# Performance work log

Hardware: AMD Instinct MI355X
Metric: run time of the kernel (lower is better)

Reference implementation:

```python
import jax, jax.numpy as jnp
import numpy as np

T, B, D, H, N, A = 128, 32, 512, 512, 64, 32  # time, batch, feat, hidden(=entry), mem_cap, anchors
TAU = 1.0

def setup_inputs() -> dict:
    key = jax.random.key(0)
    ks = jax.random.split(key, 12)
    s = 0.08  # init_scale
    u = lambda k, sh: jax.random.uniform(k, sh, jnp.float32, -s, s)
    return {
        "x": jax.random.normal(ks[0], (T, B, D), jnp.float32),
        "length": jax.random.randint(ks[1], (B,), 0, T).astype(jnp.int32),
        "u_noise": jax.random.uniform(ks[2], (T, B, N), jnp.float32),
        "W_ih": u(ks[3], (D, 3 * H)),
        "W_hh": u(ks[4], (H, 3 * H)),
        "bias": jnp.zeros((6 * H,), jnp.float32),
        "W_im": u(ks[5], (D, H)),
        "W_hm": u(ks[6], (H, H)),
        "W_um": u(ks[7], (N, H)),
        "fc1_w": u(ks[8], (H, N)),
        "fc1_b": jnp.zeros((N,), jnp.float32),
        "fc2_w": u(ks[9], (2 * H, H)),
        "fc2_b": jnp.zeros((H,), jnp.float32),
        "fc_w": u(ks[10], (H, A)),
        "fc_b": jnp.zeros((A,), jnp.float32),
    }


def reference(x, length, u_noise, W_ih, W_hh, bias, W_im, W_hm, W_um,
              fc1_w, fc1_b, fc2_w, fc2_b, fc_w, fc_b):
    bias_ih, bias_hh = bias[: 3 * H], bias[3 * H :]

    def step(carry, inp):
        h, mem, usage, last_read = carry  # h:[B,H] mem:[B,N,H] usage,last_read:[B,N]
        x_t, u_t, t = inp
        # --- write h_0 into memory (sequential fill, then overwrite last read slot)
        fill = jnp.broadcast_to(jax.nn.one_hot(t, N, dtype=h.dtype), (B, N))
        w = jnp.where(t < N, fill, last_read)
        mem = mem * (1.0 - w[:, :, None]) + w[:, :, None] * h[:, None, :]
        # --- addressing (inputs detached in original)
        last_use = jax.lax.stop_gradient(jax.nn.sigmoid(usage))
        xd = jax.lax.stop_gradient(x_t)
        hd = jax.lax.stop_gradient(h)
        read_head = jnp.tanh(xd @ W_im + hd @ W_hm + last_use @ W_um) @ fc1_w + fc1_b
        # --- gumbel softmax (hard, straight-through); noise as in original formula
        g = -jnp.log(1e-20 - jnp.log(1e-20 + u_t))
        y = jax.nn.softmax((read_head + g) * TAU, axis=1)
        hard = jax.nn.one_hot(jnp.argmax(y, axis=1), N, dtype=y.dtype)
        y_st = jax.lax.stop_gradient(hard - y) + y
        entry = jnp.einsum('bn,bnh->bh', y_st, mem)  # hard gather w/ ST grad
        # usage: add_(-1) then add_(-usage*read_index) => (usage-1)*(1-read_index)
        usage = jax.lax.stop_gradient((usage - 1.0) * (1.0 - hard))
        # --- GRU-like update with h_new from read entry
        h_new = jnp.concatenate([entry, h], axis=1) @ fc2_w + fc2_b
        wi = x_t @ W_ih + bias_ih
        wh = h_new @ W_hh + bias_hh
        ri, zi, ni = jnp.split(wi, 3, axis=1)
        rh, zh, nh = jnp.split(wh, 3, axis=1)
        r = jax.nn.sigmoid(ri + rh)
        z = jax.nn.sigmoid(zi + zh)
        n = jnp.tanh(ni + r * nh)
        h1 = (1.0 - z) * n + z * h_new
        mask = (t < length).astype(h1.dtype)[:, None]
        h1 = h1 * mask + h * (1.0 - mask)
        return (h1, mem, usage, hard), h1

    carry0 = (
        jnp.zeros((B, H), x.dtype),
        jnp.zeros((B, N, H), x.dtype),
        jnp.full((B, N), -99999.0, x.dtype),
        jnp.zeros((B, N), x.dtype),
    )
    ts = jnp.arange(T)
    _, hs = jax.lax.scan(step, carry0, (x, u_noise, ts))  # hs: [T,B,H]
    return hs @ fc_w + fc_b  # [T,B,A]
```

## Files before the change

### kernel.cpp

```cpp
#include <hip/hip_runtime.h>
#include <hip/hip_bf16.h>
#include <math.h>

#define NTHR  512
#define NBLK  256
#define HTXS  18432

#define OFF_HTX  8192
#define OFF_OC   (OFF_HTX + 129*HTXS)
#define OFF_HNEW (OFF_OC + 32*4608)
#define OFF_WHH  (OFF_HNEW + 32*64*512)
#define OFF_C0   (OFF_WHH + 32*64*1536)
#define OFF_WCAT (OFF_C0 + 1536)
#define OFF_WB16 (OFF_WCAT + 576*4608)
#define OFF_P1   (OFF_WB16 + 512*1536)
#define OFF_P2   (OFF_P1 + 4096*1536)

__device__ __forceinline__ float cohLoad(const float* p) {
  return __hip_atomic_load(p, __ATOMIC_RELAXED, __HIP_MEMORY_SCOPE_AGENT);
}
__device__ __forceinline__ void cohStore(float* p, float v) {
  __hip_atomic_store(p, v, __ATOMIC_RELAXED, __HIP_MEMORY_SCOPE_AGENT);
}
__device__ __forceinline__ int cohLoadI(const int* p) {
  return __hip_atomic_load(p, __ATOMIC_RELAXED, __HIP_MEMORY_SCOPE_AGENT);
}
__device__ __forceinline__ void cohStoreI(int* p, int v) {
  __hip_atomic_store(p, v, __ATOMIC_RELAXED, __HIP_MEMORY_SCOPE_AGENT);
}
__device__ __forceinline__ float bf2f(unsigned short u) {
  return __uint_as_float(((unsigned int)u) << 16);
}

__global__ __launch_bounds__(256) void gemm_f32(
    const float* __restrict__ A, const float* __restrict__ B,
    const float* __restrict__ bias, float* __restrict__ C,
    int M, int N, int K, int lda, int ldb, int ldc)
{
  __shared__ float As[16][132];
  __shared__ float Bs[16][64];
  const int bm = blockIdx.x * 128, bn = blockIdx.y * 64;
  const int tid = threadIdx.x;
  const int tx = tid & 15, ty = tid >> 4;
  float acc[8][4];
  #pragma unroll
  for (int i = 0; i < 8; ++i)
    #pragma unroll
    for (int j = 0; j < 4; ++j) acc[i][j] = 0.f;

  for (int kt = 0; kt < K; kt += 16) {
    #pragma unroll
    for (int i = 0; i < 2; ++i) {
      int li = tid + i*256;
      int r = li >> 2, q = li & 3;
      float4 a4 = *(const float4*)(A + (size_t)(bm + r)*lda + kt + q*4);
      As[q*4+0][r] = a4.x; As[q*4+1][r] = a4.y;
      As[q*4+2][r] = a4.z; As[q*4+3][r] = a4.w;
    }
    {
      int k = tid >> 4, nq = tid & 15;
      *(float4*)(&Bs[k][nq*4]) = *(const float4*)(B + (size_t)(kt + k)*ldb + bn + nq*4);
    }
    __syncthreads();
    #pragma unroll
    for (int kk = 0; kk < 16; ++kk) {
      float av[8], bv[4];
      *(float4*)(av)   = *(const float4*)(&As[kk][ty*8]);
      *(float4*)(av+4) = *(const float4*)(&As[kk][ty*8+4]);
      *(float4*)(bv)   = *(const float4*)(&Bs[kk][tx*4]);
      #pragma unroll
      for (int i = 0; i < 8; ++i)
        #pragma unroll
        for (int j = 0; j < 4; ++j) acc[i][j] += av[i]*bv[j];
    }
    __syncthreads();
  }
  #pragma unroll
  for (int i = 0; i < 8; ++i) {
    int m = bm + ty*8 + i;
    #pragma unroll
    for (int j = 0; j < 4; ++j) {
      int n = bn + tx*4 + j;
      float v = acc[i][j];
      if (bias) v += bias[n];
      C[(size_t)m*ldc + n] = v;
    }
  }
}

__global__ __launch_bounds__(512) void setup_kernel(
    const float* __restrict__ W_hm, const float* __restrict__ fc2_w,
    const float* __restrict__ W_um, const float* __restrict__ W_hh,
    const float* __restrict__ bias, const float* __restrict__ fc2_b,
    float* __restrict__ Wcat, float* __restrict__ c0)
{
  const int idx = blockIdx.x * 512 + threadIdx.x;
  if (idx < 512*1536) {
    int k = idx / 1536, c = idx % 1536;
    float v;
    if (c < 512)       v = W_hm[k*512 + c];
    else if (c < 1024) v = fc2_w[k*512 + (c-512)];
    else               v = fc2_w[(size_t)(512+k)*512 + (c-1024)];
    Wcat[(size_t)k*4608 + c] = v;
    return;
  }
  int i = idx - 512*1536;
  if (i < 64*4608) {
    int k2 = i / 4608, c = i % 4608;
    Wcat[(size_t)(512+k2)*4608 + c] = (c < 512) ? W_um[k2*512 + c] : 0.f;
    return;
  }
  i -= 64*4608;
  if (i < 1536) {
    float s = bias[1536 + i];
    for (int m = 0; m < 512; ++m) s += fc2_b[m] * W_hh[(size_t)m*1536 + i];
    c0[i] = s;
  }
}

__global__ __launch_bounds__(512) void cvt_kernel(
    const float* __restrict__ Wcat, unsigned short* __restrict__ Wb16)
{
  const int idx = blockIdx.x * 512 + threadIdx.x;
  const int k = idx / 3072, c = idx % 3072;
  __hip_bfloat16 h = __float2bfloat16(Wcat[(size_t)k*4608 + 1536 + c]);
  Wb16[idx] = *(unsigned short*)&h;
}

__global__ __launch_bounds__(NTHR, 1) void persist_kernel(
    const float* __restrict__ P1, const float* __restrict__ P2,
    const float* __restrict__ Wcat, const unsigned short* __restrict__ Wb16,
    float* __restrict__ oc, float* __restrict__ hTx_all,
    float* __restrict__ hnew_part, float* __restrict__ whh_part,
    const float* __restrict__ c0, const float* __restrict__ fc1_w,
    const float* __restrict__ fc1_b, const float* __restrict__ fc2_b,
    const float* __restrict__ u_noise, const int* __restrict__ length,
    const float* __restrict__ fc_w, const float* __restrict__ fc_b,
    float* __restrict__ out, int* __restrict__ bar)
{
  __shared__ float smem[13696];
  const int bid = blockIdx.x;
  const int tid = threadIdx.x;

  if (bid >= 32) {
    const int gb = bid - 32;
    const int bg = gb & 1;
    const int wv = tid >> 6, lane = tid & 63;
    const int bq = tid & 3;
    float* hxs = smem;

    if (gb < 64) {
      const int cg = gb >> 1;
      const int colbase = cg * 16;
      const int s = tid >> 5;
      const int c = (tid >> 2) & 7;
      const int kbase = s * 36;
      const float* wbase = Wcat + (size_t)kbase*4608 + colbase + c*2;
      float* red = smem + 9280;
      for (int t = 0; t < 128; ++t) {
        if (tid < 16) {
          while (cohLoadI(&bar[(bg*16 + tid)*32]) < t) __builtin_amdgcn_s_sleep(1);
        }
        __syncthreads();
        {
          const float* hsrc = hTx_all + (size_t)t*HTXS + (size_t)(bg*16)*576 + wv*72;
          float* hdst = hxs + wv*72;
          for (int i = lane; i < 288; i += 64) {
            int bb = i / 18, q = i - bb*18;
            *(float4*)(hdst + bb*580 + q*4) = *(const float4*)(hsrc + bb*576 + q*4);
          }
        }
        float acc[4][2] = {{0.f,0.f},{0.f,0.f},{0.f,0.f},{0.f,0.f}};
        const float* hp = hxs + (bq*4)*580 + kbase;
        #pragma unroll 3
        for (int it = 0; it < 9; ++it) {
          float ha[4][4];
          *(float4*)(&ha[0][0]) = *(const float4*)(hp + 0*580 + it*4);
          *(float4*)(&ha[1][0]) = *(const float4*)(hp + 1*580 + it*4);
          *(float4*)(&ha[2][0]) = *(const float4*)(hp + 2*580 + it*4);
          *(float4*)(&ha[3][0]) = *(const float4*)(hp + 3*580 + it*4);
          const float* wp = wbase + (size_t)(it*4)*4608;
          #pragma unroll
          for (int kk = 0; kk < 4; ++kk) {
            float w0 = wp[0], w1 = wp[1]; wp += 4608;
            #pragma unroll
            for (int j = 0; j < 4; ++j) {
              acc[j][0] += ha[j][kk]*w0;
              acc[j][1] += ha[j][kk]*w1;
            }
          }
        }
        {
          float* rp = red + s*272 + (bq*4)*16 + c*2;
          #pragma unroll
          for (int j = 0; j < 4; ++j)
            *(float2*)(rp + j*16) = make_float2(acc[j][0], acc[j][1]);
        }
        __syncthreads();
        if (tid < 256) {
          float ssum = 0.f;
          #pragma unroll
          for (int w = 0; w < 16; ++w) ssum += red[w*272 + tid];
          int b16 = tid >> 4, cc = tid & 15;
          cohStore(&oc[(size_t)(bg*16 + b16)*4608 + colbase + cc], ssum);
        }
        __syncthreads();
        if (tid == 0) cohStoreI(&bar[1024 + gb*32], t + 1);
      }
    } else if (gb < 128) {
      const int cg = (gb - 64) >> 1;
      const int colbase = 512 + cg * 32;
      const int s = tid >> 6;
      const int c = (tid >> 2) & 15;
      const int kbase = s * 72;
      const float* wbase = Wcat + (size_t)kbase*4608 + colbase + c*2;
      float* red = smem + 9280;
      for (int t = 0; t < 128; ++t) {
        if (tid < 16) {
          while (cohLoadI(&bar[(bg*16 + tid)*32]) < t) __builtin_amdgcn_s_sleep(1);
        }
        __syncthreads();
        {
          const float* hsrc = hTx_all + (size_t)t*HTXS + (size_t)(bg*16)*576 + wv*72;
          float* hdst = hxs + wv*72;
          for (int i = lane; i < 288; i += 64) {
            int bb = i / 18, q = i - bb*18;
            *(float4*)(hdst + bb*580 + q*4) = *(const float4*)(hsrc + bb*576 + q*4);
          }
        }
        float acc[4][2] = {{0.f,0.f},{0.f,0.f},{0.f,0.f},{0.f,0.f}};
        const float* hp = hxs + (bq*4)*580 + kbase;
        #pragma unroll 3
        for (int it = 0; it < 18; ++it) {
          float ha[4][4];
          *(float4*)(&ha[0][0]) = *(const float4*)(hp + 0*580 + it*4);
          *(float4*)(&ha[1][0]) = *(const float4*)(hp + 1*580 + it*4);
          *(float4*)(&ha[2][0]) = *(const float4*)(hp + 2*580 + it*4);
          *(float4*)(&ha[3][0]) = *(const float4*)(hp + 3*580 + it*4);
          const float* wp = wbase + (size_t)(it*4)*4608;
          #pragma unroll
          for (int kk = 0; kk < 4; ++kk) {
            float w0 = wp[0], w1 = wp[1]; wp += 4608;
            #pragma unroll
            for (int j = 0; j < 4; ++j) {
              acc[j][0] += ha[j][kk]*w0;
              acc[j][1] += ha[j][kk]*w1;
            }
          }
        }
        {
          float* rp = red + s*520 + (bq*4)*32 + c*2;
          #pragma unroll
          for (int j = 0; j < 4; ++j)
            *(float2*)(rp + j*32) = make_float2(acc[j][0], acc[j][1]);
        }
        __syncthreads();
        {
          float ssum = 0.f;
          #pragma unroll
          for (int w = 0; w < 8; ++w) ssum += red[w*520 + tid];
          int b16 = tid >> 5, cc = tid & 31;
          cohStore(&oc[(size_t)(bg*16 + b16)*4608 + colbase + cc], ssum);
        }
        __syncthreads();
        if (tid == 0) cohStoreI(&bar[1024 + gb*32], t + 1);
      }
    } else {
      const int cg = (gb - 128) >> 1;
      const int colbase = 1536 + cg * 64;
      const int s = tid >> 6;
      const int c = (tid >> 2) & 15;
      const int kbase = s * 64;
      const unsigned short* wbase = Wb16 + (size_t)kbase*3072 + (colbase - 1536) + c*4;
      float* red = smem;
      for (int t = 0; t < 128; ++t) {
        if (tid < 16) {
          while (cohLoadI(&bar[(bg*16 + tid)*32]) < t) __builtin_amdgcn_s_sleep(1);
        }
        __syncthreads();
        {
          const float* hsrc = hTx_all + (size_t)t*HTXS + (size_t)(bg*16)*576 + wv*64;
          float* hdst = hxs + wv*64;
          for (int i = lane; i < 256; i += 64) {
            int bb = i >> 4, q = i & 15;
            *(float4*)(hdst + bb*580 + q*4) = *(const float4*)(hsrc + bb*576 + q*4);
          }
        }
        float acc[4][4] = {{0.f,0.f,0.f,0.f},{0.f,0.f,0.f,0.f},
                           {0.f,0.f,0.f,0.f},{0.f,0.f,0.f,0.f}};
        const float* hp = hxs + (bq*4)*580 + kbase;
        #pragma unroll 2
        for (int it = 0; it < 16; ++it) {
          float ha[4][4];
          *(float4*)(&ha[0][0]) = *(const float4*)(hp + 0*580 + it*4);
          *(float4*)(&ha[1][0]) = *(const float4*)(hp + 1*580 + it*4);
          *(float4*)(&ha[2][0]) = *(const float4*)(hp + 2*580 + it*4);
          *(float4*)(&ha[3][0]) = *(const float4*)(hp + 3*580 + it*4);
          #pragma unroll
          for (int kk = 0; kk < 4; ++kk) {
            const ushort4 u4 = *(const ushort4*)(wbase + (size_t)(it*4 + kk)*3072);
            float w0 = bf2f(u4.x), w1 = bf2f(u4.y), w2 = bf2f(u4.z), w3 = bf2f(u4.w);
            #pragma unroll
            for (int j = 0; j < 4; ++j) {
              float f = ha[j][kk];
              acc[j][0] += f*w0; acc[j][1] += f*w1;
              acc[j][2] += f*w2; acc[j][3] += f*w3;
            }
          }
        }
        __syncthreads();
        {
          float* rp = red + s*1024 + (bq*4)*64 + c*4;
          #pragma unroll
          for (int j = 0; j < 4; ++j)
            *(float4*)(rp + j*64) = make_float4(acc[j][0], acc[j][1], acc[j][2], acc[j][3]);
        }
        __syncthreads();
        for (int i = tid; i < 1024; i += NTHR) {
          float ssum = 0.f;
          #pragma unroll
          for (int w = 0; w < 8; ++w) ssum += red[w*1024 + i];
          int b16 = i >> 6, cc = i & 63;
          cohStore(&oc[(size_t)(bg*16 + b16)*4608 + colbase + cc], ssum);
        }
        __syncthreads();
        if (tid == 0) cohStoreI(&bar[1024 + gb*32], t + 1);
      }
    }
  } else {
    const int b = bid;
    const int lenb = length[b];
    float hcur = 0.f;
    float usage_r = -99999.f;
    int jprev = 0;
    int* flg = (int*)(smem + 1100);
    const float c0r = c0[tid], c0z = c0[512 + tid], c0n = c0[1024 + tid];
    const float fc2bv = fc2_b[tid];
    const float f1b = (tid < 64) ? fc1_b[tid] : 0.f;
    const int n_ = tid & 63, kg_ = tid >> 6;
    const float* fw = fc1_w + (size_t)kg_*64*64 + n_;

    for (int t = 0; t < 128; ++t) {
      const int t32b = t*32 + b;
      const float* p1p = P1 + (size_t)t32b*1536;
      float p1r = p1p[tid], p1z = p1p[512 + tid], p1n = p1p[1024 + tid];
      float p2v = P2[(size_t)t32b*512 + tid];
      float uval = (tid < 64) ? u_noise[(size_t)t32b*64 + tid] : 0.f;
      if (tid < 64) {
        while (cohLoadI(&bar[1024 + tid*32]) < t + 1) __builtin_amdgcn_s_sleep(1);
      }
      __syncthreads();
      const float* ocb = oc + (size_t)b*4608;
      float oct = cohLoad(ocb + tid);
      smem[tid] = tanhf(p2v + oct);
      __syncthreads();
      {
        float sdot = 0.f;
        #pragma unroll 8
        for (int k = 0; k < 64; ++k) sdot += smem[kg_*64 + k] * fw[(size_t)k*64];
        smem[512 + tid] = sdot;
      }
      __syncthreads();
      if (tid < 64) {
        float l = f1b;
        #pragma unroll
        for (int kg = 0; kg < 8; ++kg) l += smem[512 + kg*64 + tid];
        l += -logf(1e-20f - logf(1e-20f + uval));
        float best = l; int idx = tid;
        #pragma unroll
        for (int off = 32; off >= 1; off >>= 1) {
          float ob = __shfl_xor(best, off);
          int   oi = __shfl_xor(idx,  off);
          if (ob > best || (ob == best && oi < idx)) { best = ob; idx = oi; }
        }
        if (tid == 0) {
          flg[0] = idx;
          flg[1] = (t < 64) ? t : jprev;
          jprev = idx;
        }
      }
      if (tid < 160) {
        while (cohLoadI(&bar[1024 + (64 + tid)*32]) < t + 1) __builtin_amdgcn_s_sleep(1);
      }
      __syncthreads();
      const int jj = flg[0], ss = flg[1];
      float vA   = cohLoad(ocb + 512  + tid);
      float vB   = cohLoad(ocb + 1024 + tid);
      float vAW0 = cohLoad(ocb + 1536 + tid);
      float vAW1 = cohLoad(ocb + 2048 + tid);
      float vAW2 = cohLoad(ocb + 2560 + tid);
      float vBW0 = cohLoad(ocb + 3072 + tid);
      float vBW1 = cohLoad(ocb + 3584 + tid);
      float vBW2 = cohLoad(ocb + 4096 + tid);
      float hnp, w0, w1, w2;
      if (jj == ss) { hnp = vA; w0 = vAW0; w1 = vAW1; w2 = vAW2; }
      else {
        hnp = hnew_part[(size_t)(b*64 + jj)*512 + tid];
        const float* wpp = whh_part + (size_t)(b*64 + jj)*1536;
        w0 = wpp[tid]; w1 = wpp[512 + tid]; w2 = wpp[1024 + tid];
      }
      float h_new = hnp + vB + fc2bv;
      float wh_r = w0 + vBW0 + c0r;
      float wh_z = w1 + vBW1 + c0z;
      float wh_n = w2 + vBW2 + c0n;
      float r  = 1.f / (1.f + expf(-(p1r + wh_r)));
      float z  = 1.f / (1.f + expf(-(p1z + wh_z)));
      float nn = tanhf(p1n + r*wh_n);
      float h1 = (1.f - z)*nn + z*h_new;
      if (t >= lenb) h1 = hcur;
      hcur = h1;
      float* hw = hTx_all + (size_t)(t + 1)*HTXS + (size_t)b*576;
      cohStore(&hw[tid], h1);
      if (tid < 64) {
        float un = (usage_r - 1.f) * (tid == jj ? 0.f : 1.f);
        usage_r = un;
        cohStore(&hw[512 + tid], 1.f / (1.f + expf(-un)));
      }
      smem[tid] = h1;
      __syncthreads();
      if (tid == 0) cohStoreI(&bar[b*32], t + 1);
      hnew_part[(size_t)(b*64 + ss)*512 + tid] = vA;
      float* wps = whh_part + (size_t)(b*64 + ss)*1536;
      wps[tid] = vAW0; wps[512 + tid] = vAW1; wps[1024 + tid] = vAW2;
      {
        int a = tid & 31, jg = tid >> 5;
        float sp = 0.f;
        #pragma unroll 8
        for (int jx = 0; jx < 32; ++jx)
          sp += smem[jg*32 + jx] * fc_w[(size_t)(jg*32 + jx)*32 + a];
        smem[512 + tid] = sp;
      }
      __syncthreads();
      if (tid < 32) {
        float s2 = fc_b[tid];
        #pragma unroll
        for (int jg = 0; jg < 16; ++jg) s2 += smem[512 + jg*32 + tid];
        out[(size_t)t32b*32 + tid] = s2;
      }
    }
  }
}

extern "C" void kernel_launch(void* const* d_in, const int* in_sizes, int n_in,
                              void* d_out, int out_size, void* d_ws, size_t ws_size,
                              hipStream_t stream)
{
  const float* x      = (const float*)d_in[0];
  const int*   length = (const int*)  d_in[1];
  const float* u_nois = (const float*)d_in[2];
  const float* W_ih   = (const float*)d_in[3];
  const float* W_hh   = (const float*)d_in[4];
  const float* bias   = (const float*)d_in[5];
  const float* W_im   = (const float*)d_in[6];
  const float* W_hm   = (const float*)d_in[7];
  const float* W_um   = (const float*)d_in[8];
  const float* fc1_w  = (const float*)d_in[9];
  const float* fc1_b  = (const float*)d_in[10];
  const float* fc2_w  = (const float*)d_in[11];
  const float* fc2_b  = (const float*)d_in[12];
  const float* fc_w   = (const float*)d_in[13];
  const float* fc_b   = (const float*)d_in[14];
  float* out = (float*)d_out;

  float* ws   = (float*)d_ws;
  int*   bar  = (int*)d_ws;
  float* hTx  = ws + OFF_HTX;
  float* oc   = ws + OFF_OC;
  float* hnew = ws + OFF_HNEW;
  float* whh  = ws + OFF_WHH;
  float* c0   = ws + OFF_C0;
  float* Wcat = ws + OFF_WCAT;
  unsigned short* Wb16 = (unsigned short*)(ws + OFF_WB16);
  float* P1   = ws + OFF_P1;
  float* P2   = ws + OFF_P2;

  hipMemsetAsync(d_ws, 0, (size_t)(OFF_HTX + HTXS) * sizeof(float), stream);
  hipMemsetAsync(hnew, 0, (size_t)(32*64*512 + 32*64*1536) * sizeof(float), stream);

  setup_kernel<<<2115, 512, 0, stream>>>(W_hm, fc2_w, W_um, W_hh, bias, fc2_b,
                                         Wcat, c0);

  { dim3 g(4, 24);
    gemm_f32<<<g, 256, 0, stream>>>(fc2_w,                   W_hh, nullptr, Wcat + 1536,
                                    512, 1536, 512, 512, 1536, 4608);
    gemm_f32<<<g, 256, 0, stream>>>(fc2_w + (size_t)512*512, W_hh, nullptr, Wcat + 3072,
                                    512, 1536, 512, 512, 1536, 4608); }
  cvt_kernel<<<3072, 512, 0, stream>>>(Wcat, Wb16);
  { dim3 g(32, 24);
    gemm_f32<<<g, 256, 0, stream>>>(x, W_ih, bias, P1, 4096, 1536, 512, 512, 1536, 1536); }
  { dim3 g(32, 8);
    gemm_f32<<<g, 256, 0, stream>>>(x, W_im, nullptr, P2, 4096, 512, 512, 512, 512, 512); }

  persist_kernel<<<NBLK, NTHR, 0, stream>>>(P1, P2, Wcat, Wb16, oc, hTx, hnew,
                                            whh, c0, fc1_w, fc1_b, fc2_b,
                                            u_nois, length, fc_w, fc_b, out, bar);
}
```

Measured before the change: 1.540 ms.

## Fuse tanh and fc1 partial dot into producer blocks; split waits to prefetch

The producer blocks that compute the read-head pre-activation columns now apply tanh with P2 themselves and multiply by their slice of fc1_w. They write 32 partial logits per batch row into a new workspace buffer, so each per-batch consumer block only sums partials instead of doing the tanh and the 512x64 matvec on its critical path. The consumer also loads the candidate hnew and whh entries unconditionally and splits the barrier wait into two groups, so those loads and the vA and vB reads overlap with the slower producers. In exchange the producers do extra work and there is an extra sync and more global traffic.

```diff
diff --git a/kernel.cpp b/kernel.cpp
--- a/kernel.cpp
+++ b/kernel.cpp
@@ -15,6 +15,7 @@
 #define OFF_WB16 (OFF_WCAT + 576*4608)
 #define OFF_P1   (OFF_WB16 + 512*1536)
 #define OFF_P2   (OFF_P1 + 4096*1536)
+#define OFF_PART (OFF_P2 + 4096*512)
 
 __device__ __forceinline__ float cohLoad(const float* p) {
   return __hip_atomic_load(p, __ATOMIC_RELAXED, __HIP_MEMORY_SCOPE_AGENT);
@@ -136,9 +137,9 @@
     const float* __restrict__ fc1_b, const float* __restrict__ fc2_b,
     const float* __restrict__ u_noise, const int* __restrict__ length,
     const float* __restrict__ fc_w, const float* __restrict__ fc_b,
-    float* __restrict__ out, int* __restrict__ bar)
+    float* __restrict__ out, int* __restrict__ bar, float* __restrict__ part)
 {
-  __shared__ float smem[13696];
+  __shared__ float smem[13952];
   const int bid = blockIdx.x;
   const int tid = threadIdx.x;
 
@@ -157,7 +158,12 @@
       const int kbase = s * 36;
       const float* wbase = Wcat + (size_t)kbase*4608 + colbase + c*2;
       float* red = smem + 9280;
+      float* thL = smem + 13632;
+      const int pb16 = tid >> 5, pn2 = (tid & 31)*2;
       for (int t = 0; t < 128; ++t) {
+        float p2v = 0.f;
+        if (tid < 256)
+          p2v = P2[(size_t)(t*32 + bg*16 + (tid>>4))*512 + colbase + (tid&15)];
         if (tid < 16) {
           while (cohLoadI(&bar[(bg*16 + tid)*32]) < t) __builtin_amdgcn_s_sleep(1);
         }
@@ -201,8 +207,19 @@
           float ssum = 0.f;
           #pragma unroll
           for (int w = 0; w < 16; ++w) ssum += red[w*272 + tid];
-          int b16 = tid >> 4, cc = tid & 15;
-          cohStore(&oc[(size_t)(bg*16 + b16)*4608 + colbase + cc], ssum);
+          thL[tid] = tanhf(p2v + ssum);
+        }
+        __syncthreads();
+        {
+          float s0 = 0.f, s1 = 0.f;
+          #pragma unroll
+          for (int k = 0; k < 16; ++k) {
+            float th = thL[pb16*16 + k];
+            const float* fw = fc1_w + (size_t)(colbase + k)*64 + pn2;
+            s0 += th * fw[0]; s1 += th * fw[1];
+          }
+          float* pp = part + (size_t)(bg*16 + pb16)*2048 + cg*64 + pn2;
+          cohStore(pp, s0); cohStore(pp + 1, s1);
         }
         __syncthreads();
         if (tid == 0) cohStoreI(&bar[1024 + gb*32], t + 1);
@@ -333,38 +350,31 @@
     float hcur = 0.f;
     float usage_r = -99999.f;
     int jprev = 0;
-    int* flg = (int*)(smem + 1100);
+    int* flg = (int*)(smem + 2176);
     const float c0r = c0[tid], c0z = c0[512 + tid], c0n = c0[1024 + tid];
     const float fc2bv = fc2_b[tid];
     const float f1b = (tid < 64) ? fc1_b[tid] : 0.f;
-    const int n_ = tid & 63, kg_ = tid >> 6;
-    const float* fw = fc1_w + (size_t)kg_*64*64 + n_;
+    const float* pbase = part + (size_t)b*2048;
 
     for (int t = 0; t < 128; ++t) {
       const int t32b = t*32 + b;
       const float* p1p = P1 + (size_t)t32b*1536;
       float p1r = p1p[tid], p1z = p1p[512 + tid], p1n = p1p[1024 + tid];
-      float p2v = P2[(size_t)t32b*512 + tid];
       float uval = (tid < 64) ? u_noise[(size_t)t32b*64 + tid] : 0.f;
       if (tid < 64) {
         while (cohLoadI(&bar[1024 + tid*32]) < t + 1) __builtin_amdgcn_s_sleep(1);
       }
       __syncthreads();
-      const float* ocb = oc + (size_t)b*4608;
-      float oct = cohLoad(ocb + tid);
-      smem[tid] = tanhf(p2v + oct);
-      __syncthreads();
       {
-        float sdot = 0.f;
-        #pragma unroll 8
-        for (int k = 0; k < 64; ++k) sdot += smem[kg_*64 + k] * fw[(size_t)k*64];
-        smem[512 + tid] = sdot;
+        const float* pp = pbase + tid*4;
+        float v0 = cohLoad(pp), v1 = cohLoad(pp+1), v2 = cohLoad(pp+2), v3 = cohLoad(pp+3);
+        *(float4*)(smem + tid*4) = make_float4(v0, v1, v2, v3);
       }
       __syncthreads();
       if (tid < 64) {
         float l = f1b;
         #pragma unroll
-        for (int kg = 0; kg < 8; ++kg) l += smem[512 + kg*64 + tid];
+        for (int g = 0; g < 32; ++g) l += smem[g*64 + tid];
         l += -logf(1e-20f - logf(1e-20f + uval));
         float best = l; int idx = tid;
         #pragma unroll
@@ -379,13 +389,21 @@
           jprev = idx;
         }
       }
-      if (tid < 160) {
+      if (tid < 64) {
         while (cohLoadI(&bar[1024 + (64 + tid)*32]) < t + 1) __builtin_amdgcn_s_sleep(1);
       }
       __syncthreads();
       const int jj = flg[0], ss = flg[1];
-      float vA   = cohLoad(ocb + 512  + tid);
-      float vB   = cohLoad(ocb + 1024 + tid);
+      const float* ocb = oc + (size_t)b*4608;
+      float hnp_c = hnew_part[(size_t)(b*64 + jj)*512 + tid];
+      const float* wpp = whh_part + (size_t)(b*64 + jj)*1536;
+      float w0_c = wpp[tid], w1_c = wpp[512 + tid], w2_c = wpp[1024 + tid];
+      float vA = cohLoad(ocb + 512  + tid);
+      float vB = cohLoad(ocb + 1024 + tid);
+      if (tid < 96) {
+        while (cohLoadI(&bar[1024 + (128 + tid)*32]) < t + 1) __builtin_amdgcn_s_sleep(1);
+      }
+      __syncthreads();
       float vAW0 = cohLoad(ocb + 1536 + tid);
       float vAW1 = cohLoad(ocb + 2048 + tid);
       float vAW2 = cohLoad(ocb + 2560 + tid);
@@ -394,11 +412,7 @@
       float vBW2 = cohLoad(ocb + 4096 + tid);
       float hnp, w0, w1, w2;
       if (jj == ss) { hnp = vA; w0 = vAW0; w1 = vAW1; w2 = vAW2; }
-      else {
-        hnp = hnew_part[(size_t)(b*64 + jj)*512 + tid];
-        const float* wpp = whh_part + (size_t)(b*64 + jj)*1536;
-        w0 = wpp[tid]; w1 = wpp[512 + tid]; w2 = wpp[1024 + tid];
-      }
+      else          { hnp = hnp_c; w0 = w0_c; w1 = w1_c; w2 = w2_c; }
       float h_new = hnp + vB + fc2bv;
       float wh_r = w0 + vBW0 + c0r;
       float wh_z = w1 + vBW1 + c0z;
@@ -473,6 +487,7 @@
   unsigned short* Wb16 = (unsigned short*)(ws + OFF_WB16);
   float* P1   = ws + OFF_P1;
   float* P2   = ws + OFF_P2;
+  float* part = ws + OFF_PART;
 
   hipMemsetAsync(d_ws, 0, (size_t)(OFF_HTX + HTXS) * sizeof(float), stream);
   hipMemsetAsync(hnew, 0, (size_t)(32*64*512 + 32*64*1536) * sizeof(float), stream);
@@ -493,5 +508,6 @@
 
   persist_kernel<<<NBLK, NTHR, 0, stream>>>(P1, P2, Wcat, Wb16, oc, hTx, hnew,
                                             whh, c0, fc1_w, fc1_b, fc2_b,
-                                            u_nois, length, fc_w, fc_b, out, bar);
-}
+                                            u_nois, length, fc_w, fc_b, out, bar,
+                                            part);
+}
```

Measured after the change: 1.601 ms. +3.9%, slower.

## Rebalance column-group block partitioning across worker blocks in persistent kernel

Applied to the files above, without the earlier changes.

Removes the dedicated 16-column worker class for the first 512 output columns. The first 96 worker blocks now cover columns 0-1535 in 32-column groups, and the bf16 blocks cover 48 columns each instead of 64. The batch blocks' barrier waits are adjusted to match: they wait on 32 blocks before the read head and 192 blocks before the gather. The goal is to shorten the critical path, since the read-head logits now depend on fewer producer blocks, and to even out per-block work. In exchange it uses scalar 3-wide weight loads and an unaligned reduction layout in the bf16 blocks.

```diff
diff --git a/kernel.cpp b/kernel.cpp
--- a/kernel.cpp
+++ b/kernel.cpp
@@ -149,67 +149,9 @@
     const int bq = tid & 3;
     float* hxs = smem;
 
-    if (gb < 64) {
+    if (gb < 96) {
       const int cg = gb >> 1;
-      const int colbase = cg * 16;
-      const int s = tid >> 5;
-      const int c = (tid >> 2) & 7;
-      const int kbase = s * 36;
-      const float* wbase = Wcat + (size_t)kbase*4608 + colbase + c*2;
-      float* red = smem + 9280;
-      for (int t = 0; t < 128; ++t) {
-        if (tid < 16) {
-          while (cohLoadI(&bar[(bg*16 + tid)*32]) < t) __builtin_amdgcn_s_sleep(1);
-        }
-        __syncthreads();
-        {
-          const float* hsrc = hTx_all + (size_t)t*HTXS + (size_t)(bg*16)*576 + wv*72;
-          float* hdst = hxs + wv*72;
-          for (int i = lane; i < 288; i += 64) {
-            int bb = i / 18, q = i - bb*18;
-            *(float4*)(hdst + bb*580 + q*4) = *(const float4*)(hsrc + bb*576 + q*4);
-          }
-        }
-        float acc[4][2] = {{0.f,0.f},{0.f,0.f},{0.f,0.f},{0.f,0.f}};
-        const float* hp = hxs + (bq*4)*580 + kbase;
-        #pragma unroll 3
-        for (int it = 0; it < 9; ++it) {
-          float ha[4][4];
-          *(float4*)(&ha[0][0]) = *(const float4*)(hp + 0*580 + it*4);
-          *(float4*)(&ha[1][0]) = *(const float4*)(hp + 1*580 + it*4);
-          *(float4*)(&ha[2][0]) = *(const float4*)(hp + 2*580 + it*4);
-          *(float4*)(&ha[3][0]) = *(const float4*)(hp + 3*580 + it*4);
-          const float* wp = wbase + (size_t)(it*4)*4608;
-          #pragma unroll
-          for (int kk = 0; kk < 4; ++kk) {
-            float w0 = wp[0], w1 = wp[1]; wp += 4608;
-            #pragma unroll
-            for (int j = 0; j < 4; ++j) {
-              acc[j][0] += ha[j][kk]*w0;
-              acc[j][1] += ha[j][kk]*w1;
-            }
-          }
-        }
-        {
-          float* rp = red + s*272 + (bq*4)*16 + c*2;
-          #pragma unroll
-          for (int j = 0; j < 4; ++j)
-            *(float2*)(rp + j*16) = make_float2(acc[j][0], acc[j][1]);
-        }
-        __syncthreads();
-        if (tid < 256) {
-          float ssum = 0.f;
-          #pragma unroll
-          for (int w = 0; w < 16; ++w) ssum += red[w*272 + tid];
-          int b16 = tid >> 4, cc = tid & 15;
-          cohStore(&oc[(size_t)(bg*16 + b16)*4608 + colbase + cc], ssum);
-        }
-        __syncthreads();
-        if (tid == 0) cohStoreI(&bar[1024 + gb*32], t + 1);
-      }
-    } else if (gb < 128) {
-      const int cg = (gb - 64) >> 1;
-      const int colbase = 512 + cg * 32;
+      const int colbase = cg * 32;
       const int s = tid >> 6;
       const int c = (tid >> 2) & 15;
       const int kbase = s * 72;
@@ -266,12 +208,12 @@
         if (tid == 0) cohStoreI(&bar[1024 + gb*32], t + 1);
       }
     } else {
-      const int cg = (gb - 128) >> 1;
-      const int colbase = 1536 + cg * 64;
+      const int cg = (gb - 96) >> 1;
+      const int colbase = 1536 + cg * 48;
       const int s = tid >> 6;
       const int c = (tid >> 2) & 15;
       const int kbase = s * 64;
-      const unsigned short* wbase = Wb16 + (size_t)kbase*3072 + (colbase - 1536) + c*4;
+      const unsigned short* wbase = Wb16 + (size_t)kbase*3072 + (colbase - 1536) + c*3;
       float* red = smem;
       for (int t = 0; t < 128; ++t) {
         if (tid < 16) {
@@ -286,8 +228,7 @@
             *(float4*)(hdst + bb*580 + q*4) = *(const float4*)(hsrc + bb*576 + q*4);
           }
         }
-        float acc[4][4] = {{0.f,0.f,0.f,0.f},{0.f,0.f,0.f,0.f},
-                           {0.f,0.f,0.f,0.f},{0.f,0.f,0.f,0.f}};
+        float acc[4][3] = {{0.f,0.f,0.f},{0.f,0.f,0.f},{0.f,0.f,0.f},{0.f,0.f,0.f}};
         const float* hp = hxs + (bq*4)*580 + kbase;
         #pragma unroll 2
         for (int it = 0; it < 16; ++it) {
@@ -298,29 +239,31 @@
           *(float4*)(&ha[3][0]) = *(const float4*)(hp + 3*580 + it*4);
           #pragma unroll
           for (int kk = 0; kk < 4; ++kk) {
-            const ushort4 u4 = *(const ushort4*)(wbase + (size_t)(it*4 + kk)*3072);
-            float w0 = bf2f(u4.x), w1 = bf2f(u4.y), w2 = bf2f(u4.z), w3 = bf2f(u4.w);
+            const unsigned short* wp = wbase + (size_t)(it*4 + kk)*3072;
+            float w0 = bf2f(wp[0]), w1 = bf2f(wp[1]), w2 = bf2f(wp[2]);
             #pragma unroll
             for (int j = 0; j < 4; ++j) {
               float f = ha[j][kk];
-              acc[j][0] += f*w0; acc[j][1] += f*w1;
-              acc[j][2] += f*w2; acc[j][3] += f*w3;
+              acc[j][0] += f*w0; acc[j][1] += f*w1; acc[j][2] += f*w2;
             }
           }
         }
         __syncthreads();
         {
-          float* rp = red + s*1024 + (bq*4)*64 + c*4;
-          #pragma unroll
-          for (int j = 0; j < 4; ++j)
-            *(float4*)(rp + j*64) = make_float4(acc[j][0], acc[j][1], acc[j][2], acc[j][3]);
-        }
-        __syncthreads();
-        for (int i = tid; i < 1024; i += NTHR) {
+          float* rp = red + s*776 + (bq*4)*48 + c*3;
+          #pragma unroll
+          for (int j = 0; j < 4; ++j) {
+            rp[j*48 + 0] = acc[j][0];
+            rp[j*48 + 1] = acc[j][1];
+            rp[j*48 + 2] = acc[j][2];
+          }
+        }
+        __syncthreads();
+        for (int i = tid; i < 768; i += NTHR) {
           float ssum = 0.f;
           #pragma unroll
-          for (int w = 0; w < 8; ++w) ssum += red[w*1024 + i];
-          int b16 = i >> 6, cc = i & 63;
+          for (int w = 0; w < 8; ++w) ssum += red[w*776 + i];
+          int b16 = i / 48, cc = i - b16*48;
           cohStore(&oc[(size_t)(bg*16 + b16)*4608 + colbase + cc], ssum);
         }
         __syncthreads();
@@ -346,7 +289,7 @@
       float p1r = p1p[tid], p1z = p1p[512 + tid], p1n = p1p[1024 + tid];
       float p2v = P2[(size_t)t32b*512 + tid];
       float uval = (tid < 64) ? u_noise[(size_t)t32b*64 + tid] : 0.f;
-      if (tid < 64) {
+      if (tid < 32) {
         while (cohLoadI(&bar[1024 + tid*32]) < t + 1) __builtin_amdgcn_s_sleep(1);
       }
       __syncthreads();
@@ -379,8 +322,8 @@
           jprev = idx;
         }
       }
-      if (tid < 160) {
-        while (cohLoadI(&bar[1024 + (64 + tid)*32]) < t + 1) __builtin_amdgcn_s_sleep(1);
+      if (tid < 192) {
+        while (cohLoadI(&bar[1024 + (32 + tid)*32]) < t + 1) __builtin_amdgcn_s_sleep(1);
       }
       __syncthreads();
       const int jj = flg[0], ss = flg[1];
```

Result: slower. 1.901 ms (+23.4%).
